# Optimization experiments

Measured on AMD Instinct MI355X. Metric: run time of the kernel, lower is better.

## Reference

```python
import jax, jax.numpy as jnp
import numpy as np
import math

D_EMBED = 1536
N_HEADS = 12
D_AUG = D_EMBED // 3          # 512
HEAD_DIM = D_EMBED // N_HEADS # 128
ROPE_BASE = 10000.0


def apply_rope(x):
    # x: [B, S, H, D], interleaved-pair RoPE (torchtune convention)
    B, S, H, D = x.shape
    half = D // 2
    freqs = 1.0 / (ROPE_BASE ** (jnp.arange(0, D, 2, dtype=jnp.float32) / D))  # [half]
    ang = jnp.arange(S, dtype=jnp.float32)[:, None] * freqs[None, :]           # [S, half]
    cos = jnp.cos(ang)[None, :, None, :]  # [1,S,1,half]
    sin = jnp.sin(ang)[None, :, None, :]
    xr = x.reshape(B, S, H, half, 2)
    x1, x2 = xr[..., 0], xr[..., 1]
    out = jnp.stack([x1 * cos - x2 * sin, x1 * sin + x2 * cos], axis=-1)
    return out.reshape(B, S, H, D).astype(x.dtype)


def setup_inputs() -> dict:
    key = jax.random.key(0)
    ks = jax.random.split(key, 7)
    B, S = 2, 2048
    s = 0.02
    return {
        "q": jax.random.normal(ks[0], (B, S, D_EMBED), jnp.float32),
        "k": jax.random.normal(ks[1], (B, S, D_EMBED), jnp.float32),
        "v": jax.random.normal(ks[2], (B, S, D_EMBED), jnp.float32),
        "W_q": jax.random.normal(ks[3], (D_EMBED, D_EMBED), jnp.float32) * s,
        "W_k": jax.random.normal(ks[4], (D_EMBED, D_EMBED), jnp.float32) * s,
        "W_v": jax.random.normal(ks[5], (D_AUG, D_AUG), jnp.float32) * s,
        "W_o": jax.random.normal(ks[6], (D_EMBED, D_EMBED), jnp.float32) * s,
    }


def reference(q, k, v, W_q, W_k, W_v, W_o):
    # Dropout layers are identity in eval mode.
    B, S, _ = q.shape
    qh = q @ W_q.T                                     # [B,S,D]
    kh = k @ W_k.T
    v_mid = v[:, :, D_AUG:2 * D_AUG] @ W_v.T           # [B,S,D_AUG]
    vh = jnp.concatenate(
        [v_mid, jnp.zeros_like(v_mid), jnp.zeros_like(v_mid)], axis=-1)  # [B,S,D]

    qh = qh.reshape(B, S, N_HEADS, HEAD_DIM)
    kh = kh.reshape(B, S, N_HEADS, HEAD_DIM)
    vh = vh.reshape(B, S, N_HEADS, HEAD_DIM)

    qh = apply_rope(qh)
    kh = apply_rope(kh)

    scores = jnp.einsum('bqhd,bkhd->bhqk', qh, kh) / math.sqrt(HEAD_DIM)
    causal = jnp.triu(jnp.ones((S, S), dtype=bool), k=1)
    scores = jnp.where(causal[None, None], -jnp.inf, scores)
    probs = jax.nn.softmax(scores, axis=-1)

    attn = jnp.einsum('bhqk,bkhd->bqhd', probs, vh).reshape(B, S, D_EMBED)
    return attn @ W_o.T
```

## Files before the change

### kernel.cpp

```cpp
#include <hip/hip_runtime.h>
#include <hip/hip_bf16.h>

typedef __attribute__((ext_vector_type(8))) short short8;
typedef __attribute__((ext_vector_type(4))) short short4v;
typedef __attribute__((ext_vector_type(4))) float f32x4;

__device__ __forceinline__ short f2bf(float f) {
    union { float f; unsigned u; } v; v.f = f;
    unsigned r = (v.u + 0x7fffu + ((v.u >> 16) & 1u)) >> 16;
    return (short)r;
}
__device__ __forceinline__ float bf2f(short s) {
    union { unsigned u; float f; } v; v.u = ((unsigned)(unsigned short)s) << 16;
    return v.f;
}
__device__ __forceinline__ f32x4 zero4() { f32x4 z = {0.f, 0.f, 0.f, 0.f}; return z; }

__device__ __forceinline__ void gl16(const void* g, void* l) {
    __builtin_amdgcn_global_load_lds(
        (const __attribute__((address_space(1))) void*)g,
        (__attribute__((address_space(3))) void*)l, 16, 0, 0);
}

__global__ __launch_bounds__(256) void convertA_kernel(
    const float* __restrict__ q, const float* __restrict__ k,
    const float* __restrict__ Wq, const float* __restrict__ Wk,
    short* __restrict__ qb, short* __restrict__ kb,
    short* __restrict__ Wqb, short* __restrict__ Wkb)
{
    const int e0 = (blockIdx.x * 256 + threadIdx.x) * 8;
    const float* src; short* dst; int n;
    switch (blockIdx.z) {
    case 0:  n = 6291456; src = q + e0;  dst = qb;  break;
    case 1:  n = 6291456; src = k + e0;  dst = kb;  break;
    case 2:  n = 786432;  src = Wq + e0; dst = Wqb; break;
    default: n = 786432;  src = Wk + e0; dst = Wkb; break;
    }
    if (e0 >= n) return;
    float4 f0 = ((const float4*)src)[0];
    float4 f1 = ((const float4*)src)[1];
    short8 o;
    o[0]=f2bf(f0.x); o[1]=f2bf(f0.y); o[2]=f2bf(f0.z); o[3]=f2bf(f0.w);
    o[4]=f2bf(f1.x); o[5]=f2bf(f1.y); o[6]=f2bf(f1.z); o[7]=f2bf(f1.w);
    *(short8*)(dst + e0) = o;
}

__global__ __launch_bounds__(256) void convertB_kernel(
    const float* __restrict__ Wo, short* __restrict__ Wob)
{
    const int e0 = (blockIdx.x * 256 + threadIdx.x) * 8;
    const float* src = Wo + (size_t)(e0 >> 9) * 1536 + (e0 & 511);
    float4 f0 = ((const float4*)src)[0];
    float4 f1 = ((const float4*)src)[1];
    short8 o;
    o[0]=f2bf(f0.x); o[1]=f2bf(f0.y); o[2]=f2bf(f0.z); o[3]=f2bf(f0.w);
    o[4]=f2bf(f1.x); o[5]=f2bf(f1.y); o[6]=f2bf(f1.z); o[7]=f2bf(f1.w);
    *(short8*)(Wob + e0) = o;
}

template<int STORE>
__device__ __forceinline__ void gemm97(
    const short* __restrict__ A, const short* __restrict__ B, void* __restrict__ Cp,
    int K, int lda, int ldb, int ldc, short* As, short* Bs)
{
    const int bm = blockIdx.y * 128;
    const int bn = blockIdx.x * 128;
    const int tid = threadIdx.x;
    const int w = tid >> 6;
    const int lane = tid & 63;
    const int l15 = lane & 15;
    const int quad = lane >> 4;
    const int wm = (w >> 1) * 64;
    const int wn = (w & 1) * 64;

    const int srow = w * 32 + (lane >> 2);
    const int scol = (lane & 3) * 8;
    const short* ga = A + (size_t)(bm + srow) * lda + scol;
    const short* gb = B + (size_t)(bn + srow) * ldb + scol;
    short* laA0 = &As[(w * 32) * 32];
    short* laA1 = &As[(w * 32 + 16) * 32];
    short* laB0 = &Bs[(w * 32) * 32];
    short* laB1 = &Bs[(w * 32 + 16) * 32];

    f32x4 acc[4][4];
#pragma unroll
    for (int i = 0; i < 4; i++)
#pragma unroll
        for (int j = 0; j < 4; j++) acc[i][j] = zero4();

    for (int k0 = 0; k0 < K; k0 += 32) {
        __syncthreads();
        gl16(ga + k0, laA0);
        gl16(ga + k0 + (size_t)16 * lda, laA1);
        gl16(gb + k0, laB0);
        gl16(gb + k0 + (size_t)16 * ldb, laB1);
        __syncthreads();

        short8 af[4], bf[4];
#pragma unroll
        for (int i = 0; i < 4; i++)
            af[i] = *(const short8*)&As[(wm + i * 16 + l15) * 32 + quad * 8];
#pragma unroll
        for (int j = 0; j < 4; j++)
            bf[j] = *(const short8*)&Bs[(wn + j * 16 + l15) * 32 + quad * 8];
#pragma unroll
        for (int i = 0; i < 4; i++)
#pragma unroll
            for (int j = 0; j < 4; j++)
                acc[i][j] = __builtin_amdgcn_mfma_f32_16x16x32_bf16(af[i], bf[j], acc[i][j], 0, 0, 0);
    }

#pragma unroll
    for (int i = 0; i < 4; i++)
#pragma unroll
        for (int j = 0; j < 4; j++) {
            const int col = bn + wn + j * 16 + l15;
            const int row0 = bm + wm + i * 16 + quad * 4;
#pragma unroll
            for (int r = 0; r < 4; r++) {
                if constexpr (STORE == 0)
                    ((short*)Cp)[(size_t)(row0 + r) * ldc + col] = f2bf(acc[i][j][r]);
                else
                    ((float*)Cp)[(size_t)(row0 + r) * ldc + col] = acc[i][j][r];
            }
        }
}

__device__ __forceinline__ void gemm_f32_bt_T(
    const float* __restrict__ A, const float* __restrict__ Bw, short* __restrict__ Cp,
    int K, int lda, int ldb, int ldc, short* As, short* Bs)
{
    const int bm = blockIdx.y * 128;
    const int bn = blockIdx.x * 128;
    const int tid = threadIdx.x;
    const int w = tid >> 6;
    const int lane = tid & 63;
    const int l15 = lane & 15;
    const int quad = lane >> 4;
    const int wm = (w >> 1) * 64;
    const int wn = (w & 1) * 64;
    const int srow = tid >> 1;
    const int scol = (tid & 1) * 16;

    f32x4 acc[4][4];
#pragma unroll
    for (int i = 0; i < 4; i++)
#pragma unroll
        for (int j = 0; j < 4; j++) acc[i][j] = zero4();

    for (int k0 = 0; k0 < K; k0 += 32) {
        __syncthreads();
        {
            const float* src = A + (size_t)(bm + srow) * lda + k0 + scol;
            short* dst = &As[srow * 40 + scol];
            const float4* s4 = (const float4*)src;
            float4 f0 = s4[0], f1 = s4[1], f2 = s4[2], f3 = s4[3];
            short8 t0, t1;
            t0[0]=f2bf(f0.x); t0[1]=f2bf(f0.y); t0[2]=f2bf(f0.z); t0[3]=f2bf(f0.w);
            t0[4]=f2bf(f1.x); t0[5]=f2bf(f1.y); t0[6]=f2bf(f1.z); t0[7]=f2bf(f1.w);
            t1[0]=f2bf(f2.x); t1[1]=f2bf(f2.y); t1[2]=f2bf(f2.z); t1[3]=f2bf(f2.w);
            t1[4]=f2bf(f3.x); t1[5]=f2bf(f3.y); t1[6]=f2bf(f3.z); t1[7]=f2bf(f3.w);
            *(short8*)dst = t0; *(short8*)(dst + 8) = t1;
        }
        {
            const float* src = Bw + (size_t)(bn + srow) * ldb + k0 + scol;
            short* dst = &Bs[srow * 40 + scol];
            const float4* s4 = (const float4*)src;
            float4 f0 = s4[0], f1 = s4[1], f2 = s4[2], f3 = s4[3];
            short8 t0, t1;
            t0[0]=f2bf(f0.x); t0[1]=f2bf(f0.y); t0[2]=f2bf(f0.z); t0[3]=f2bf(f0.w);
            t0[4]=f2bf(f1.x); t0[5]=f2bf(f1.y); t0[6]=f2bf(f1.z); t0[7]=f2bf(f1.w);
            t1[0]=f2bf(f2.x); t1[1]=f2bf(f2.y); t1[2]=f2bf(f2.z); t1[3]=f2bf(f2.w);
            t1[4]=f2bf(f3.x); t1[5]=f2bf(f3.y); t1[6]=f2bf(f3.z); t1[7]=f2bf(f3.w);
            *(short8*)dst = t0; *(short8*)(dst + 8) = t1;
        }
        __syncthreads();

        short8 af[4], bfr[4];
#pragma unroll
        for (int i = 0; i < 4; i++)
            af[i] = *(const short8*)&As[(wm + i * 16 + l15) * 40 + quad * 8];
#pragma unroll
        for (int j = 0; j < 4; j++)
            bfr[j] = *(const short8*)&Bs[(wn + j * 16 + l15) * 40 + quad * 8];
#pragma unroll
        for (int i = 0; i < 4; i++)
#pragma unroll
            for (int j = 0; j < 4; j++)
                acc[i][j] = __builtin_amdgcn_mfma_f32_16x16x32_bf16(af[i], bfr[j], acc[i][j], 0, 0, 0);
    }

#pragma unroll
    for (int i = 0; i < 4; i++)
#pragma unroll
        for (int j = 0; j < 4; j++) {
            const int col = bn + wn + j * 16 + l15;
            const int row0 = bm + wm + i * 16 + quad * 4;
            short4v p;
#pragma unroll
            for (int r = 0; r < 4; r++) p[r] = f2bf(acc[i][j][r]);
            *(short4v*)&Cp[(size_t)col * ldc + row0] = p;
        }
}

__global__ __launch_bounds__(256) void proj_kernel(
    const short* __restrict__ qb, const short* __restrict__ kb, const float* __restrict__ v,
    const short* __restrict__ Wqb, const short* __restrict__ Wkb, const float* __restrict__ Wv,
    short* __restrict__ qh, short* __restrict__ kh, short* __restrict__ vT)
{
    __shared__ short smem[2][5120];
    switch (blockIdx.z) {
    case 0:  gemm97<0>(qb, Wqb, qh, 1536, 1536, 1536, 512, smem[0], smem[1]); break;
    case 1:  gemm97<0>(kb, Wkb, kh, 1536, 1536, 1536, 512, smem[0], smem[1]); break;
    default: gemm_f32_bt_T(v + 512, Wv, vT, 512, 1536, 512, 4096, smem[0], smem[1]); break;
    }
}

__global__ __launch_bounds__(256) void outproj_kernel(
    const short* __restrict__ attn, const short* __restrict__ Wob, float* __restrict__ out)
{
    __shared__ short smem[2][4096];
    gemm97<2>(attn, Wob, out, 512, 512, 512, 1536, smem[0], smem[1]);
}

__global__ __launch_bounds__(256) void rope_kernel(short* __restrict__ qh, short* __restrict__ kh)
{
    short* buf = blockIdx.z ? kh : qh;
    const int e0 = (blockIdx.x * 256 + threadIdx.x) * 8;
    const int row = e0 >> 9;
    const int c0 = e0 & 511;
    const float pos = (float)(row & 2047);
    short8 xv = *(short8*)&buf[e0];
    short8 ov;
#pragma unroll
    for (int p = 0; p < 4; p++) {
        const int pair = ((c0 + 2 * p) & 127) >> 1;
        const float freq = exp2f(-(float)(2 * pair) * (13.287712379549449f / 128.0f));
        const float ang = pos * freq;
        const float n = rintf(ang * 0.15915494309189535f);
        const float r = (ang - n * 6.28125f) - n * 1.9353071795864769e-3f;
        float s, c;
        __sincosf(r, &s, &c);
        const float x1 = bf2f(xv[2 * p]), x2 = bf2f(xv[2 * p + 1]);
        ov[2 * p]     = f2bf(x1 * c - x2 * s);
        ov[2 * p + 1] = f2bf(x1 * s + x2 * c);
    }
    *(short8*)&buf[e0] = ov;
}

__global__ __launch_bounds__(256) void flash_kernel(
    const short* __restrict__ qh, const short* __restrict__ kh,
    const short* __restrict__ vT, short* __restrict__ attn)
{
    __shared__ float Os[4][16][128];
    __shared__ short Ps[4][16 * 40];
    __shared__ float Ms[64], Lp[64];

    const int id = blockIdx.x;
    const int hb = id & 7;
    const int b = hb & 1;
    const int h = hb >> 1;
    const int qt = 127 - (id >> 3);
    const int q0 = qt * 16;
    const int tid = threadIdx.x;
    const int w = tid >> 6;
    const int lane = tid & 63;
    const int l15 = lane & 15;
    const int quad = lane >> 4;

    const short* qrow = qh + (size_t)(b * 2048 + q0 + l15) * 512 + h * 128;
    short8 aq[4];
#pragma unroll
    for (int kk = 0; kk < 4; kk++)
        aq[kk] = *(const short8*)&qrow[kk * 32 + quad * 8];

    f32x4 o[8];
#pragma unroll
    for (int dt = 0; dt < 8; dt++) o[dt] = zero4();
    float mrow[4], lrow[4];
#pragma unroll
    for (int r = 0; r < 4; r++) { mrow[r] = -1e30f; lrow[r] = 0.0f; }

    const float scale = 0.08838834764831845f;
    const int ntiles = (q0 + 47) >> 5;
    const short* kbp = kh + (size_t)(b * 2048) * 512 + h * 128;
    const short* vbp = vT + (size_t)(h * 128) * 4096 + b * 2048;
    short* pw = &Ps[w][0];

    for (int t = w; t < ntiles; t += 4) {
        const int kb0 = t * 32;

        f32x4 sc[2];
#pragma unroll
        for (int ct = 0; ct < 2; ct++) {
            sc[ct] = zero4();
            const short* kr = kbp + (size_t)(kb0 + ct * 16 + l15) * 512;
#pragma unroll
            for (int kk = 0; kk < 4; kk++) {
                short8 bk = *(const short8*)&kr[kk * 32 + quad * 8];
                sc[ct] = __builtin_amdgcn_mfma_f32_16x16x32_bf16(aq[kk], bk, sc[ct], 0, 0, 0);
            }
        }

        short8 bv[8];
#pragma unroll
        for (int dt = 0; dt < 8; dt++)
            bv[dt] = *(const short8*)&vbp[(size_t)(dt * 16 + l15) * 4096 + kb0 + quad * 8];

        const int rbase = q0 + quad * 4;
        float s[2][4];
#pragma unroll
        for (int ct = 0; ct < 2; ct++) {
            const int kcol = kb0 + ct * 16 + l15;
#pragma unroll
            for (int r = 0; r < 4; r++) {
                float vv = sc[ct][r] * scale;
                s[ct][r] = (kcol > rbase + r) ? -1e30f : vv;
            }
        }

#pragma unroll
        for (int r = 0; r < 4; r++) {
            float mx = fmaxf(s[0][r], s[1][r]);
#pragma unroll
            for (int off = 1; off < 16; off <<= 1)
                mx = fmaxf(mx, __shfl_xor(mx, off, 64));
            const float mnew = fmaxf(mrow[r], mx);
            const float alpha = __expf(mrow[r] - mnew);
            float p0 = __expf(s[0][r] - mnew);
            float p1 = __expf(s[1][r] - mnew);
            s[0][r] = p0; s[1][r] = p1;
            float psum = p0 + p1;
#pragma unroll
            for (int off = 1; off < 16; off <<= 1)
                psum += __shfl_xor(psum, off, 64);
            lrow[r] = alpha * lrow[r] + psum;
            mrow[r] = mnew;
#pragma unroll
            for (int dt = 0; dt < 8; dt++) o[dt][r] *= alpha;
        }

#pragma unroll
        for (int ct = 0; ct < 2; ct++)
#pragma unroll
            for (int r = 0; r < 4; r++)
                pw[(quad * 4 + r) * 40 + ct * 16 + l15] = f2bf(s[ct][r]);
        short8 ap = *(const short8*)&pw[l15 * 40 + quad * 8];

#pragma unroll
        for (int dt = 0; dt < 8; dt++)
            o[dt] = __builtin_amdgcn_mfma_f32_16x16x32_bf16(ap, bv[dt], o[dt], 0, 0, 0);
    }

    if (l15 == 0) {
#pragma unroll
        for (int r = 0; r < 4; r++) Ms[w * 16 + quad * 4 + r] = mrow[r];
    }
    __syncthreads();
#pragma unroll
    for (int r = 0; r < 4; r++) {
        const int row = quad * 4 + r;
        float gm = fmaxf(fmaxf(Ms[row], Ms[16 + row]), fmaxf(Ms[32 + row], Ms[48 + row]));
        const float f = __expf(mrow[r] - gm);
        if (l15 == 0) Lp[w * 16 + row] = lrow[r] * f;
#pragma unroll
        for (int dt = 0; dt < 8; dt++)
            Os[w][row][dt * 16 + l15] = o[dt][r] * f;
    }
    __syncthreads();

    {
        const int row = tid >> 4;
        const int d0 = (tid & 15) * 8;
        const float rL = 1.0f / (Lp[row] + Lp[16 + row] + Lp[32 + row] + Lp[48 + row]);
        short8 ov;
#pragma unroll
        for (int j = 0; j < 8; j++) {
            const float osum = Os[0][row][d0 + j] + Os[1][row][d0 + j]
                             + Os[2][row][d0 + j] + Os[3][row][d0 + j];
            ov[j] = f2bf(osum * rL);
        }
        *(short8*)&attn[(size_t)(b * 2048 + q0 + row) * 512 + h * 128 + d0] = ov;
    }
}

extern "C" void kernel_launch(void* const* d_in, const int* in_sizes, int n_in,
                              void* d_out, int out_size, void* d_ws, size_t ws_size,
                              hipStream_t stream) {
    const float* q  = (const float*)d_in[0];
    const float* k  = (const float*)d_in[1];
    const float* v  = (const float*)d_in[2];
    const float* Wq = (const float*)d_in[3];
    const float* Wk = (const float*)d_in[4];
    const float* Wv = (const float*)d_in[5];
    const float* Wo = (const float*)d_in[6];
    float* out = (float*)d_out;

    const size_t MB = 1024 * 1024;
    char* ws = (char*)d_ws;
    short* qh   = (short*)(ws);
    short* kh   = (short*)(ws + 4 * MB);
    short* vT   = (short*)(ws + 8 * MB);
    short* Wqb  = (short*)(ws + 12 * MB);
    short* Wkb  = (short*)(ws + 13 * MB + 512 * 1024);
    short* attn = (short*)(ws + 12 * MB);
    short* Wob  = (short*)(ws);
    short* qb   = (short*)d_out;
    short* kb   = (short*)((char*)d_out + 12 * MB);

    convertA_kernel<<<dim3(3072, 1, 4), 256, 0, stream>>>(q, k, Wq, Wk, qb, kb, Wqb, Wkb);
    proj_kernel<<<dim3(4, 32, 3), 256, 0, stream>>>(qb, kb, v, Wqb, Wkb, Wv, qh, kh, vT);
    rope_kernel<<<dim3(1024, 1, 2), 256, 0, stream>>>(qh, kh);
    flash_kernel<<<dim3(1024, 1, 1), 256, 0, stream>>>(qh, kh, vT, attn);
    convertB_kernel<<<dim3(384, 1, 1), 256, 0, stream>>>(Wo, Wob);
    outproj_kernel<<<dim3(12, 32, 1), 256, 0, stream>>>(attn, Wob, out);
}
```

Measured before the change: 265.1 us.

## Split flash attention KV tiles across eight waves with LDS tree reduction

Doubles the flash kernel's block to 512 threads, so eight waves each take every eighth KV tile instead of four waves each taking every fourth. The cross-wave merge of the partial outputs becomes a log-step tree reduction through shared memory rather than a four-way sum. The P staging buffer now shares storage with the reduction buffer to keep shared-memory use low. The aim is more latency hiding and shorter per-wave serial loops, at the cost of extra barriers and reduction traffic, and idle waves for short causal rows.

```diff
diff --git a/kernel.cpp b/kernel.cpp
--- a/kernel.cpp
+++ b/kernel.cpp
@@ -248,13 +248,13 @@
     *(short8*)&buf[e0] = ov;
 }
 
-__global__ __launch_bounds__(256) void flash_kernel(
+__global__ __launch_bounds__(512) void flash_kernel(
     const short* __restrict__ qh, const short* __restrict__ kh,
     const short* __restrict__ vT, short* __restrict__ attn)
 {
-    __shared__ float Os[4][16][128];
-    __shared__ short Ps[4][16 * 40];
-    __shared__ float Ms[64], Lp[64];
+    __shared__ float Osf[4 * 2048];
+    __shared__ float Ms[128], Lp[128];
+    short* Ps = (short*)Osf;
 
     const int id = blockIdx.x;
     const int hb = id & 7;
@@ -285,9 +285,9 @@
     const int ntiles = (q0 + 47) >> 5;
     const short* kbp = kh + (size_t)(b * 2048) * 512 + h * 128;
     const short* vbp = vT + (size_t)(h * 128) * 4096 + b * 2048;
-    short* pw = &Ps[w][0];
-
-    for (int t = w; t < ntiles; t += 4) {
+    short* pw = &Ps[w * 640];
+
+    for (int t = w; t < ntiles; t += 8) {
         const int kb0 = t * 32;
 
         f32x4 sc[2];
@@ -357,30 +357,51 @@
         for (int r = 0; r < 4; r++) Ms[w * 16 + quad * 4 + r] = mrow[r];
     }
     __syncthreads();
+
 #pragma unroll
     for (int r = 0; r < 4; r++) {
         const int row = quad * 4 + r;
-        float gm = fmaxf(fmaxf(Ms[row], Ms[16 + row]), fmaxf(Ms[32 + row], Ms[48 + row]));
+        float gm = Ms[row];
+#pragma unroll
+        for (int j = 1; j < 8; j++) gm = fmaxf(gm, Ms[j * 16 + row]);
         const float f = __expf(mrow[r] - gm);
         if (l15 == 0) Lp[w * 16 + row] = lrow[r] * f;
 #pragma unroll
-        for (int dt = 0; dt < 8; dt++)
-            Os[w][row][dt * 16 + l15] = o[dt][r] * f;
+        for (int dt = 0; dt < 8; dt++) o[dt][r] *= f;
     }
     __syncthreads();
 
-    {
-        const int row = tid >> 4;
-        const int d0 = (tid & 15) * 8;
-        const float rL = 1.0f / (Lp[row] + Lp[16 + row] + Lp[32 + row] + Lp[48 + row]);
-        short8 ov;
-#pragma unroll
-        for (int j = 0; j < 8; j++) {
-            const float osum = Os[0][row][d0 + j] + Os[1][row][d0 + j]
-                             + Os[2][row][d0 + j] + Os[3][row][d0 + j];
-            ov[j] = f2bf(osum * rL);
-        }
-        *(short8*)&attn[(size_t)(b * 2048 + q0 + row) * 512 + h * 128 + d0] = ov;
+#pragma unroll
+    for (int step = 4; step >= 1; step >>= 1) {
+        if (w >= step && w < 2 * step) {
+            float* dst = &Osf[(w - step) * 2048];
+#pragma unroll
+            for (int dt = 0; dt < 8; dt++)
+                *(f32x4*)&dst[(dt * 16 + l15) * 16 + quad * 4] = o[dt];
+        }
+        __syncthreads();
+        if (w < step) {
+            const float* srcp = &Osf[w * 2048];
+#pragma unroll
+            for (int dt = 0; dt < 8; dt++)
+                o[dt] += *(const f32x4*)&srcp[(dt * 16 + l15) * 16 + quad * 4];
+        }
+        __syncthreads();
+    }
+
+    if (w == 0) {
+#pragma unroll
+        for (int r = 0; r < 4; r++) {
+            const int row = quad * 4 + r;
+            float L = Lp[row];
+#pragma unroll
+            for (int j = 1; j < 8; j++) L += Lp[j * 16 + row];
+            const float rL = 1.0f / L;
+            short* orow = attn + (size_t)(b * 2048 + q0 + row) * 512 + h * 128;
+#pragma unroll
+            for (int dt = 0; dt < 8; dt++)
+                orow[dt * 16 + l15] = f2bf(o[dt][r] * rL);
+        }
     }
 }
 
@@ -411,7 +432,7 @@
     convertA_kernel<<<dim3(3072, 1, 4), 256, 0, stream>>>(q, k, Wq, Wk, qb, kb, Wqb, Wkb);
     proj_kernel<<<dim3(4, 32, 3), 256, 0, stream>>>(qb, kb, v, Wqb, Wkb, Wv, qh, kh, vT);
     rope_kernel<<<dim3(1024, 1, 2), 256, 0, stream>>>(qh, kh);
-    flash_kernel<<<dim3(1024, 1, 1), 256, 0, stream>>>(qh, kh, vT, attn);
+    flash_kernel<<<dim3(1024, 1, 1), 512, 0, stream>>>(qh, kh, vT, attn);
     convertB_kernel<<<dim3(384, 1, 1), 256, 0, stream>>>(Wo, Wob);
     outproj_kernel<<<dim3(12, 32, 1), 256, 0, stream>>>(attn, Wob, out);
 }
```

Measured after the change: 271.3 us. +2.3%, slower.

## Split flash attention along keys into chunks with a merge kernel; deepen GEMM K-step

Applied to the files above, without the earlier changes.

The attention kernel now splits each query tile's key range into up to four chunks of 16 key tiles. Each chunk runs in its own block and writes unnormalized fp16 partial outputs plus its row max and sum to scratch space in the output buffer. A new merge kernel combines the partials with log-sum-exp rescaling, which evens out the per-block work that the causal triangle makes uneven for long query tiles. Separately, the GEMM loads a 64-wide K slab per barrier pair instead of 32, halving the synchronisations at the cost of doubled LDS. The trade-offs are an extra launch, partial-result traffic, and fp16 rounding of the partial outputs.

```diff
diff --git a/kernel.cpp b/kernel.cpp
--- a/kernel.cpp
+++ b/kernel.cpp
@@ -4,6 +4,7 @@
 typedef __attribute__((ext_vector_type(8))) short short8;
 typedef __attribute__((ext_vector_type(4))) short short4v;
 typedef __attribute__((ext_vector_type(4))) float f32x4;
+typedef __attribute__((ext_vector_type(8))) _Float16 f16x8;
 
 __device__ __forceinline__ short f2bf(float f) {
     union { float f; unsigned u; } v; v.f = f;
@@ -77,10 +78,6 @@
     const int scol = (lane & 3) * 8;
     const short* ga = A + (size_t)(bm + srow) * lda + scol;
     const short* gb = B + (size_t)(bn + srow) * ldb + scol;
-    short* laA0 = &As[(w * 32) * 32];
-    short* laA1 = &As[(w * 32 + 16) * 32];
-    short* laB0 = &Bs[(w * 32) * 32];
-    short* laB1 = &Bs[(w * 32 + 16) * 32];
 
     f32x4 acc[4][4];
 #pragma unroll
@@ -88,26 +85,34 @@
 #pragma unroll
         for (int j = 0; j < 4; j++) acc[i][j] = zero4();
 
-    for (int k0 = 0; k0 < K; k0 += 32) {
+    for (int k0 = 0; k0 < K; k0 += 64) {
         __syncthreads();
-        gl16(ga + k0, laA0);
-        gl16(ga + k0 + (size_t)16 * lda, laA1);
-        gl16(gb + k0, laB0);
-        gl16(gb + k0 + (size_t)16 * ldb, laB1);
+#pragma unroll
+        for (int p = 0; p < 2; p++) {
+            gl16(ga + k0 + p * 32,                     &As[p * 4096 + (w * 32) * 32]);
+            gl16(ga + k0 + p * 32 + (size_t)16 * lda,  &As[p * 4096 + (w * 32 + 16) * 32]);
+            gl16(gb + k0 + p * 32,                     &Bs[p * 4096 + (w * 32) * 32]);
+            gl16(gb + k0 + p * 32 + (size_t)16 * ldb,  &Bs[p * 4096 + (w * 32 + 16) * 32]);
+        }
         __syncthreads();
 
-        short8 af[4], bf[4];
+        short8 af[2][4], bf[2][4];
+#pragma unroll
+        for (int p = 0; p < 2; p++) {
+#pragma unroll
+            for (int i = 0; i < 4; i++)
+                af[p][i] = *(const short8*)&As[p * 4096 + (wm + i * 16 + l15) * 32 + quad * 8];
+#pragma unroll
+            for (int j = 0; j < 4; j++)
+                bf[p][j] = *(const short8*)&Bs[p * 4096 + (wn + j * 16 + l15) * 32 + quad * 8];
+        }
 #pragma unroll
         for (int i = 0; i < 4; i++)
-            af[i] = *(const short8*)&As[(wm + i * 16 + l15) * 32 + quad * 8];
-#pragma unroll
-        for (int j = 0; j < 4; j++)
-            bf[j] = *(const short8*)&Bs[(wn + j * 16 + l15) * 32 + quad * 8];
-#pragma unroll
-        for (int i = 0; i < 4; i++)
-#pragma unroll
-            for (int j = 0; j < 4; j++)
-                acc[i][j] = __builtin_amdgcn_mfma_f32_16x16x32_bf16(af[i], bf[j], acc[i][j], 0, 0, 0);
+#pragma unroll
+            for (int j = 0; j < 4; j++) {
+                acc[i][j] = __builtin_amdgcn_mfma_f32_16x16x32_bf16(af[0][i], bf[0][j], acc[i][j], 0, 0, 0);
+                acc[i][j] = __builtin_amdgcn_mfma_f32_16x16x32_bf16(af[1][i], bf[1][j], acc[i][j], 0, 0, 0);
+            }
     }
 
 #pragma unroll
@@ -208,7 +213,7 @@
     const short* __restrict__ Wqb, const short* __restrict__ Wkb, const float* __restrict__ Wv,
     short* __restrict__ qh, short* __restrict__ kh, short* __restrict__ vT)
 {
-    __shared__ short smem[2][5120];
+    __shared__ short smem[2][8192];
     switch (blockIdx.z) {
     case 0:  gemm97<0>(qb, Wqb, qh, 1536, 1536, 1536, 512, smem[0], smem[1]); break;
     case 1:  gemm97<0>(kb, Wkb, kh, 1536, 1536, 1536, 512, smem[0], smem[1]); break;
@@ -219,7 +224,7 @@
 __global__ __launch_bounds__(256) void outproj_kernel(
     const short* __restrict__ attn, const short* __restrict__ Wob, float* __restrict__ out)
 {
-    __shared__ short smem[2][4096];
+    __shared__ short smem[2][8192];
     gemm97<2>(attn, Wob, out, 512, 512, 512, 1536, smem[0], smem[1]);
 }
 
@@ -250,7 +255,7 @@
 
 __global__ __launch_bounds__(256) void flash_kernel(
     const short* __restrict__ qh, const short* __restrict__ kh,
-    const short* __restrict__ vT, short* __restrict__ attn)
+    const short* __restrict__ vT, _Float16* __restrict__ pO, float2* __restrict__ pML)
 {
     __shared__ float Os[4][16][128];
     __shared__ short Ps[4][16 * 40];
@@ -260,8 +265,17 @@
     const int hb = id & 7;
     const int b = hb & 1;
     const int h = hb >> 1;
-    const int qt = 127 - (id >> 3);
+    const int r = id >> 3;
+    const int qt = 127 - (r >> 2);
+    const int chunk = r & 3;
+    const int m_ = qt >> 1;
+    const int ntiles = m_ + 1;
+    const int nch = (m_ + 16) >> 4;
+    if (chunk >= nch) return;
     const int q0 = qt * 16;
+    const int t0 = chunk * 16;
+    const int tend = (t0 + 16 < ntiles) ? (t0 + 16) : ntiles;
+
     const int tid = threadIdx.x;
     const int w = tid >> 6;
     const int lane = tid & 63;
@@ -279,15 +293,14 @@
     for (int dt = 0; dt < 8; dt++) o[dt] = zero4();
     float mrow[4], lrow[4];
 #pragma unroll
-    for (int r = 0; r < 4; r++) { mrow[r] = -1e30f; lrow[r] = 0.0f; }
+    for (int rr = 0; rr < 4; rr++) { mrow[rr] = -1e30f; lrow[rr] = 0.0f; }
 
     const float scale = 0.08838834764831845f;
-    const int ntiles = (q0 + 47) >> 5;
     const short* kbp = kh + (size_t)(b * 2048) * 512 + h * 128;
     const short* vbp = vT + (size_t)(h * 128) * 4096 + b * 2048;
     short* pw = &Ps[w][0];
 
-    for (int t = w; t < ntiles; t += 4) {
+    for (int t = t0 + w; t < tend; t += 4) {
         const int kb0 = t * 32;
 
         f32x4 sc[2];
@@ -313,38 +326,38 @@
         for (int ct = 0; ct < 2; ct++) {
             const int kcol = kb0 + ct * 16 + l15;
 #pragma unroll
-            for (int r = 0; r < 4; r++) {
-                float vv = sc[ct][r] * scale;
-                s[ct][r] = (kcol > rbase + r) ? -1e30f : vv;
+            for (int rr = 0; rr < 4; rr++) {
+                float vv = sc[ct][rr] * scale;
+                s[ct][rr] = (kcol > rbase + rr) ? -1e30f : vv;
             }
         }
 
 #pragma unroll
-        for (int r = 0; r < 4; r++) {
-            float mx = fmaxf(s[0][r], s[1][r]);
+        for (int rr = 0; rr < 4; rr++) {
+            float mx = fmaxf(s[0][rr], s[1][rr]);
 #pragma unroll
             for (int off = 1; off < 16; off <<= 1)
                 mx = fmaxf(mx, __shfl_xor(mx, off, 64));
-            const float mnew = fmaxf(mrow[r], mx);
-            const float alpha = __expf(mrow[r] - mnew);
-            float p0 = __expf(s[0][r] - mnew);
-            float p1 = __expf(s[1][r] - mnew);
-            s[0][r] = p0; s[1][r] = p1;
+            const float mnew = fmaxf(mrow[rr], mx);
+            const float alpha = __expf(mrow[rr] - mnew);
+            float p0 = __expf(s[0][rr] - mnew);
+            float p1 = __expf(s[1][rr] - mnew);
+            s[0][rr] = p0; s[1][rr] = p1;
             float psum = p0 + p1;
 #pragma unroll
             for (int off = 1; off < 16; off <<= 1)
                 psum += __shfl_xor(psum, off, 64);
-            lrow[r] = alpha * lrow[r] + psum;
-            mrow[r] = mnew;
-#pragma unroll
-            for (int dt = 0; dt < 8; dt++) o[dt][r] *= alpha;
+            lrow[rr] = alpha * lrow[rr] + psum;
+            mrow[rr] = mnew;
+#pragma unroll
+            for (int dt = 0; dt < 8; dt++) o[dt][rr] *= alpha;
         }
 
 #pragma unroll
         for (int ct = 0; ct < 2; ct++)
 #pragma unroll
-            for (int r = 0; r < 4; r++)
-                pw[(quad * 4 + r) * 40 + ct * 16 + l15] = f2bf(s[ct][r]);
+            for (int rr = 0; rr < 4; rr++)
+                pw[(quad * 4 + rr) * 40 + ct * 16 + l15] = f2bf(s[ct][rr]);
         short8 ap = *(const short8*)&pw[l15 * 40 + quad * 8];
 
 #pragma unroll
@@ -354,34 +367,82 @@
 
     if (l15 == 0) {
 #pragma unroll
-        for (int r = 0; r < 4; r++) Ms[w * 16 + quad * 4 + r] = mrow[r];
+        for (int rr = 0; rr < 4; rr++) Ms[w * 16 + quad * 4 + rr] = mrow[rr];
     }
     __syncthreads();
 #pragma unroll
-    for (int r = 0; r < 4; r++) {
-        const int row = quad * 4 + r;
+    for (int rr = 0; rr < 4; rr++) {
+        const int row = quad * 4 + rr;
         float gm = fmaxf(fmaxf(Ms[row], Ms[16 + row]), fmaxf(Ms[32 + row], Ms[48 + row]));
-        const float f = __expf(mrow[r] - gm);
-        if (l15 == 0) Lp[w * 16 + row] = lrow[r] * f;
+        const float f = __expf(mrow[rr] - gm);
+        if (l15 == 0) Lp[w * 16 + row] = lrow[rr] * f;
 #pragma unroll
         for (int dt = 0; dt < 8; dt++)
-            Os[w][row][dt * 16 + l15] = o[dt][r] * f;
+            Os[w][row][dt * 16 + l15] = o[dt][rr] * f;
     }
     __syncthreads();
 
     {
+        const int a = m_ >> 4, c = m_ & 15;
+        const int S = 2 * (m_ + 8 * a * (a - 1) + c * a) + (qt & 1) * (a + 1);
+        const int slot = hb * 320 + S + chunk;
+
         const int row = tid >> 4;
         const int d0 = (tid & 15) * 8;
-        const float rL = 1.0f / (Lp[row] + Lp[16 + row] + Lp[32 + row] + Lp[48 + row]);
-        short8 ov;
+        f16x8 po;
 #pragma unroll
         for (int j = 0; j < 8; j++) {
             const float osum = Os[0][row][d0 + j] + Os[1][row][d0 + j]
                              + Os[2][row][d0 + j] + Os[3][row][d0 + j];
-            ov[j] = f2bf(osum * rL);
-        }
-        *(short8*)&attn[(size_t)(b * 2048 + q0 + row) * 512 + h * 128 + d0] = ov;
-    }
+            po[j] = (_Float16)osum;
+        }
+        *(f16x8*)&pO[(size_t)slot * 2048 + row * 128 + d0] = po;
+        if ((tid & 15) == 0) {
+            const float gm = fmaxf(fmaxf(Ms[row], Ms[16 + row]), fmaxf(Ms[32 + row], Ms[48 + row]));
+            const float L = Lp[row] + Lp[16 + row] + Lp[32 + row] + Lp[48 + row];
+            pML[slot * 16 + row] = make_float2(gm, L);
+        }
+    }
+}
+
+__global__ __launch_bounds__(256) void fmerge_kernel(
+    const _Float16* __restrict__ pO, const float2* __restrict__ pML, short* __restrict__ attn)
+{
+    const int id = blockIdx.x;
+    const int hb = id & 7;
+    const int b = hb & 1;
+    const int h = hb >> 1;
+    const int qt = id >> 3;
+    const int m_ = qt >> 1;
+    const int nch = (m_ + 16) >> 4;
+    const int a = m_ >> 4, c = m_ & 15;
+    const int S = 2 * (m_ + 8 * a * (a - 1) + c * a) + (qt & 1) * (a + 1);
+    const int s0 = hb * 320 + S;
+
+    const int row = threadIdx.x >> 4;
+    const int d0 = (threadIdx.x & 15) * 8;
+
+    float M = -1e30f;
+    for (int s = 0; s < nch; s++)
+        M = fmaxf(M, pML[(s0 + s) * 16 + row].x);
+
+    float L = 0.0f;
+    float o[8];
+#pragma unroll
+    for (int j = 0; j < 8; j++) o[j] = 0.0f;
+    for (int s = 0; s < nch; s++) {
+        const float2 ml = pML[(s0 + s) * 16 + row];
+        const float f = __expf(ml.x - M);
+        L += ml.y * f;
+        f16x8 po = *(const f16x8*)&pO[(size_t)(s0 + s) * 2048 + row * 128 + d0];
+#pragma unroll
+        for (int j = 0; j < 8; j++) o[j] += f * (float)po[j];
+    }
+    const float rL = 1.0f / L;
+    short8 ov;
+#pragma unroll
+    for (int j = 0; j < 8; j++) ov[j] = f2bf(o[j] * rL);
+    *(short8*)&attn[(size_t)(b * 2048 + qt * 16 + row) * 512 + h * 128 + d0] = ov;
 }
 
 extern "C" void kernel_launch(void* const* d_in, const int* in_sizes, int n_in,
@@ -407,11 +468,14 @@
     short* Wob  = (short*)(ws);
     short* qb   = (short*)d_out;
     short* kb   = (short*)((char*)d_out + 12 * MB);
+    _Float16* pO = (_Float16*)d_out;
+    float2*  pML = (float2*)((char*)d_out + 12 * MB);
 
     convertA_kernel<<<dim3(3072, 1, 4), 256, 0, stream>>>(q, k, Wq, Wk, qb, kb, Wqb, Wkb);
     proj_kernel<<<dim3(4, 32, 3), 256, 0, stream>>>(qb, kb, v, Wqb, Wkb, Wv, qh, kh, vT);
     rope_kernel<<<dim3(1024, 1, 2), 256, 0, stream>>>(qh, kh);
-    flash_kernel<<<dim3(1024, 1, 1), 256, 0, stream>>>(qh, kh, vT, attn);
+    flash_kernel<<<dim3(4096, 1, 1), 256, 0, stream>>>(qh, kh, vT, pO, pML);
+    fmerge_kernel<<<dim3(1024, 1, 1), 256, 0, stream>>>(pO, pML, attn);
     convertB_kernel<<<dim3(384, 1, 1), 256, 0, stream>>>(Wo, Wob);
     outproj_kernel<<<dim3(12, 32, 1), 256, 0, stream>>>(attn, Wob, out);
 }
```

Result: slower. 306.9 us (+15.8%).
